# Kernel tuning notes

Measured on AMD Instinct MI355X. Metric: run time of the kernel, lower is better.

## Reference

```python
import jax, jax.numpy as jnp
import numpy as np

N_NODES = 100000
N_EDGES = 1600000
D_FEAT = 128
HIDDEN = 16
N_CLASSES = 16


def setup_inputs() -> dict:
    key = jax.random.key(0)
    ks = jax.random.split(key, 6)
    x = jax.random.normal(ks[0], (N_NODES, D_FEAT), dtype=jnp.float32)
    edge_index = jax.random.randint(ks[1], (2, N_EDGES), 0, N_NODES, dtype=jnp.int64)
    # Glorot-ish scaled weights
    w1_rel = jax.random.normal(ks[2], (D_FEAT, HIDDEN), dtype=jnp.float32) / np.sqrt(D_FEAT)
    w1_root = jax.random.normal(ks[3], (D_FEAT, HIDDEN), dtype=jnp.float32) / np.sqrt(D_FEAT)
    b1 = jnp.zeros((HIDDEN,), dtype=jnp.float32)
    w2_rel = jax.random.normal(ks[4], (HIDDEN, N_CLASSES), dtype=jnp.float32) / np.sqrt(HIDDEN)
    w2_root = jax.random.normal(ks[5], (HIDDEN, N_CLASSES), dtype=jnp.float32) / np.sqrt(HIDDEN)
    b2 = jnp.zeros((N_CLASSES,), dtype=jnp.float32)
    return {"x": x, "edge_index": edge_index, "w1_rel": w1_rel, "w1_root": w1_root,
            "b1": b1, "w2_rel": w2_rel, "w2_root": w2_root, "b2": b2}


def _graph_conv(x, src, dst, w_rel, w_root, b):
    # PyG GraphConv(aggr='add'): out_i = lin_rel(sum_{j->i} x_j) + lin_root(x_i)
    n = x.shape[0]
    agg = jax.ops.segment_sum(x[src], dst, num_segments=n)  # [N, d_in]
    return agg @ w_rel + x @ w_root + b


def reference(x, edge_index, w1_rel, w1_root, b1, w2_rel, w2_root, b2):
    src, dst = edge_index[0], edge_index[1]
    h = jax.nn.relu(_graph_conv(x, src, dst, w1_rel, w1_root, b1))
    # F.dropout(training=False) -> identity in eval mode
    out = _graph_conv(h, src, dst, w2_rel, w2_root, b2)
    return jax.nn.log_softmax(out, axis=1)
```

## Files before the change

### kernel.cpp

```cpp
#include <hip/hip_runtime.h>

#define DFEAT 128
#define HID 16
#define BKT_NODES 128
#define BKT_SHIFT 7
#define CAP 2432
#define CAPI 5
#define CHUNK 8192
#define NOEDGE 0xFFFFFFFFu

typedef __attribute__((ext_vector_type(8))) short short8;
typedef __attribute__((ext_vector_type(4))) float floatx4;

__device__ __forceinline__ float bf2f(unsigned v) { return __uint_as_float(v << 16); }
__device__ __forceinline__ unsigned short f2bf(float f) {
    unsigned u = __float_as_uint(f);
    return (unsigned short)((u + 0x7FFFu + ((u >> 16) & 1u)) >> 16);
}
__device__ __forceinline__ unsigned pack2(float a, float b) {
    return (unsigned)f2bf(a) | ((unsigned)f2bf(b) << 16);
}

__global__ __launch_bounds__(512) void k_detect(const unsigned short* __restrict__ x,
                                                const int* __restrict__ ei,
                                                int* __restrict__ flags,
                                                int* __restrict__ gcur, int nbkt) {
    const int t = threadIdx.x;
    for (int i = t; i < nbkt; i += 512) gcur[i] = 0;
    if (t < 64) {
        unsigned short v = x[2 * t];
        int e = (v >> 7) & 0xFF;
        bool okbf = (v == 0) || (e >= 110 && e <= 130);
        unsigned long long mbf = __ballot(okbf);
        bool z = (ei[2 * t + 1] == 0);
        unsigned long long mz = __ballot(z);
        if (t == 0) {
            flags[0] = (__popcll(mbf) >= 52) ? 1 : 0;
            flags[1] = (__popcll(mz) >= 60) ? 1 : 0;
        }
    }
}

__global__ __launch_bounds__(512) void k_pl(const int* __restrict__ ei,
                                            unsigned* __restrict__ eb,
                                            int* __restrict__ gcur,
                                            const void* __restrict__ xv,
                                            const void* __restrict__ wrel,
                                            const void* __restrict__ wroot,
                                            unsigned short* __restrict__ p1b,
                                            unsigned short* __restrict__ q1b,
                                            const int* __restrict__ flags,
                                            int E, int nbkt, int N, int nPart) {
    __shared__ int hist[1024];
    const int t = threadIdx.x;

    if ((int)blockIdx.x < nPart) {
        for (int i = t; i < nbkt; i += 512) hist[i] = 0;
        __syncthreads();
        const int base = blockIdx.x * CHUNK;
        const int i64 = flags[1];
        unsigned pk[16];
        unsigned bkrk[16];
        if (i64 && !(E & 1)) {
#pragma unroll
            for (int ip = 0; ip < 8; ++ip) {
                int e = base + ip * 1024 + 2 * t;
                if (e < E) {
                    int4 sv = *(const int4*)(ei + 2 * (size_t)e);
                    int4 dv = *(const int4*)(ei + 2 * ((size_t)E + e));
                    int b0 = dv.x >> BKT_SHIFT;
                    pk[2 * ip] = ((unsigned)sv.x << BKT_SHIFT) | (unsigned)(dv.x & (BKT_NODES - 1));
                    int r0 = atomicAdd(&hist[b0], 1);
                    bkrk[2 * ip] = ((unsigned)b0 << 13) | (unsigned)r0;
                    int b1 = dv.z >> BKT_SHIFT;
                    pk[2 * ip + 1] = ((unsigned)sv.z << BKT_SHIFT) | (unsigned)(dv.z & (BKT_NODES - 1));
                    int r1 = atomicAdd(&hist[b1], 1);
                    bkrk[2 * ip + 1] = ((unsigned)b1 << 13) | (unsigned)r1;
                } else {
                    bkrk[2 * ip] = NOEDGE;
                    bkrk[2 * ip + 1] = NOEDGE;
                }
            }
        } else {
#pragma unroll
            for (int i = 0; i < 16; ++i) {
                int e = base + i * 512 + t;
                if (e < E) {
                    int src, dst;
                    if (i64) { src = ei[2 * (size_t)e]; dst = ei[2 * ((size_t)E + e)]; }
                    else     { src = ei[e];             dst = ei[(size_t)E + e]; }
                    int b = dst >> BKT_SHIFT;
                    pk[i] = ((unsigned)src << BKT_SHIFT) | (unsigned)(dst & (BKT_NODES - 1));
                    int r = atomicAdd(&hist[b], 1);
                    bkrk[i] = ((unsigned)b << 13) | (unsigned)r;
                } else {
                    bkrk[i] = NOEDGE;
                }
            }
        }
        __syncthreads();
        for (int b = t; b < nbkt; b += 512) {
            int c = hist[b];
            hist[b] = c ? atomicAdd(&gcur[b], c) : 0;
        }
        __syncthreads();
#pragma unroll
        for (int i = 0; i < 16; ++i) {
            if (bkrk[i] != NOEDGE) {
                int b = (int)(bkrk[i] >> 13);
                int pos = hist[b] + (int)(bkrk[i] & 0x1FFFu);
                if (pos < CAP)
                    eb[(size_t)b * CAP + pos] = pk[i];
            }
        }
        return;
    }

    const int lane = t & 63, wave = t >> 6;
    const int bf = flags[0];
    const int m = lane & 15;
    const int quad = lane >> 4;
    const int nodebase = ((int)blockIdx.x - nPart) * 128 + wave * 16;

    short8 Brel[4], Broot[4];
    if (bf) {
        const unsigned short* a = (const unsigned short*)wrel;
        const unsigned short* c = (const unsigned short*)wroot;
#pragma unroll
        for (int kb = 0; kb < 4; ++kb) {
            short8 br, bo;
#pragma unroll
            for (int j = 0; j < 8; ++j) {
                int k = kb * 32 + quad * 8 + j;
                br[j] = (short)a[k * HID + m];
                bo[j] = (short)c[k * HID + m];
            }
            Brel[kb] = br; Broot[kb] = bo;
        }
    } else {
        const float* a = (const float*)wrel;
        const float* c = (const float*)wroot;
#pragma unroll
        for (int kb = 0; kb < 4; ++kb) {
            short8 br, bo;
#pragma unroll
            for (int j = 0; j < 8; ++j) {
                int k = kb * 32 + quad * 8 + j;
                br[j] = (short)f2bf(a[k * HID + m]);
                bo[j] = (short)f2bf(c[k * HID + m]);
            }
            Brel[kb] = br; Broot[kb] = bo;
        }
    }

    int row = nodebase + m;
    if (row >= N) row = N - 1;

    floatx4 accP = {0.f, 0.f, 0.f, 0.f}, accQ = {0.f, 0.f, 0.f, 0.f};
    if (bf) {
        const unsigned short* xp = (const unsigned short*)xv;
        const unsigned short* rp = xp + (size_t)row * DFEAT + quad * 8;
#pragma unroll
        for (int kb = 0; kb < 4; ++kb) {
            short8 A = *(const short8*)(rp + kb * 32);
            accP = __builtin_amdgcn_mfma_f32_16x16x32_bf16(A, Brel[kb], accP, 0, 0, 0);
            accQ = __builtin_amdgcn_mfma_f32_16x16x32_bf16(A, Broot[kb], accQ, 0, 0, 0);
        }
    } else {
        const float* xp = (const float*)xv;
        const float* rp = xp + (size_t)row * DFEAT + quad * 8;
#pragma unroll
        for (int kb = 0; kb < 4; ++kb) {
            float4 v0 = *(const float4*)(rp + kb * 32);
            float4 v1 = *(const float4*)(rp + kb * 32 + 4);
            short8 A;
            A[0] = (short)f2bf(v0.x); A[1] = (short)f2bf(v0.y);
            A[2] = (short)f2bf(v0.z); A[3] = (short)f2bf(v0.w);
            A[4] = (short)f2bf(v1.x); A[5] = (short)f2bf(v1.y);
            A[6] = (short)f2bf(v1.z); A[7] = (short)f2bf(v1.w);
            accP = __builtin_amdgcn_mfma_f32_16x16x32_bf16(A, Brel[kb], accP, 0, 0, 0);
            accQ = __builtin_amdgcn_mfma_f32_16x16x32_bf16(A, Broot[kb], accQ, 0, 0, 0);
        }
    }

#pragma unroll
    for (int r = 0; r < 4; ++r) {
        int node = nodebase + quad * 4 + r;
        if (node < N) {
            p1b[(size_t)node * HID + m] = f2bf(accP[r]);
            q1b[(size_t)node * HID + m] = f2bf(accQ[r]);
        }
    }
}

__global__ __launch_bounds__(512) void k_sagg1(const unsigned* __restrict__ eb,
                                               const int* __restrict__ gcur,
                                               const unsigned short* __restrict__ p1b,
                                               const unsigned short* __restrict__ q1b,
                                               const void* __restrict__ b1,
                                               const void* __restrict__ w2rel,
                                               const void* __restrict__ w2root,
                                               unsigned short* __restrict__ p2b,
                                               unsigned short* __restrict__ q2b,
                                               unsigned* __restrict__ csr,
                                               int* __restrict__ offsets,
                                               const int* __restrict__ flags,
                                               int N) {
    __shared__ unsigned srt[CAP];
    __shared__ int cnts[BKT_NODES];
    __shared__ int offs[BKT_NODES];
    __shared__ float4 swpR[HID][4];
    __shared__ float4 swpO[HID][4];
    __shared__ float sb[HID];
    const int t = threadIdx.x;
    const int b = blockIdx.x;
    const int bf = flags[0];

    if (t < 64) {
        int k = t >> 2, p = t & 3;
        float4 wr, wo;
        if (bf) {
            const unsigned short* a = (const unsigned short*)w2rel;
            const unsigned short* c = (const unsigned short*)w2root;
            wr = make_float4(bf2f(a[k * 16 + 4 * p]),     bf2f(a[k * 16 + 4 * p + 1]),
                             bf2f(a[k * 16 + 4 * p + 2]), bf2f(a[k * 16 + 4 * p + 3]));
            wo = make_float4(bf2f(c[k * 16 + 4 * p]),     bf2f(c[k * 16 + 4 * p + 1]),
                             bf2f(c[k * 16 + 4 * p + 2]), bf2f(c[k * 16 + 4 * p + 3]));
        } else {
            const float* a = (const float*)w2rel;
            const float* c = (const float*)w2root;
            wr = make_float4(a[k * 16 + 4 * p], a[k * 16 + 4 * p + 1],
                             a[k * 16 + 4 * p + 2], a[k * 16 + 4 * p + 3]);
            wo = make_float4(c[k * 16 + 4 * p], c[k * 16 + 4 * p + 1],
                             c[k * 16 + 4 * p + 2], c[k * 16 + 4 * p + 3]);
        }
        swpR[k][p] = wr;
        swpO[k][p] = wo;
    }
    if (t < HID) sb[t] = bf ? bf2f(((const unsigned short*)b1)[t]) : ((const float*)b1)[t];
    if (t < BKT_NODES) cnts[t] = 0;
    __syncthreads();

    int cnt = gcur[b];
    if (cnt < 0) cnt = 0;
    if (cnt > CAP) cnt = CAP;
    const unsigned* ep = eb + (size_t)b * CAP;

    unsigned ev[CAPI];
    int rk[CAPI];
#pragma unroll
    for (int i = 0; i < CAPI; ++i) {
        int e = i * 512 + t;
        if (e < cnt) {
            unsigned w = ep[e];
            ev[i] = w;
            rk[i] = atomicAdd(&cnts[w & (BKT_NODES - 1u)], 1);
        } else ev[i] = NOEDGE;
    }
    __syncthreads();
    if (t < BKT_NODES) offs[t] = cnts[t];
    __syncthreads();
    for (int off = 1; off < BKT_NODES; off <<= 1) {
        int v = 0;
        if (t >= off && t < BKT_NODES) v = offs[t - off];
        __syncthreads();
        if (t < BKT_NODES) offs[t] += v;
        __syncthreads();
    }
#pragma unroll
    for (int i = 0; i < CAPI; ++i) {
        if (ev[i] != NOEDGE) {
            unsigned local = ev[i] & (BKT_NODES - 1u);
            int pos = offs[local] - cnts[local] + rk[i];
            srt[pos] = ev[i] >> BKT_SHIFT;
        }
    }
    __syncthreads();

    const int base = b * CAP;
    for (int e = t; e < cnt; e += 512) csr[base + e] = srt[e];
    const int gb = b * BKT_NODES;
    if (t < BKT_NODES) {
        int gn = gb + t;
        if (gn < N) offsets[gn] = base + offs[t] - cnts[t];
    }

    const int node = t >> 2, jp = t & 3;
    const int gn = gb + node;
    const int beg = offs[node] - cnts[node];
    const int end = offs[node];
    float a0 = 0.f, a1 = 0.f, a2 = 0.f, a3 = 0.f;
    int e = beg;
    for (; e + 8 <= end; e += 8) {
        uint2 u0 = *(const uint2*)(p1b + (size_t)srt[e + 0] * HID + 4 * jp);
        uint2 u1 = *(const uint2*)(p1b + (size_t)srt[e + 1] * HID + 4 * jp);
        uint2 u2 = *(const uint2*)(p1b + (size_t)srt[e + 2] * HID + 4 * jp);
        uint2 u3 = *(const uint2*)(p1b + (size_t)srt[e + 3] * HID + 4 * jp);
        uint2 u4 = *(const uint2*)(p1b + (size_t)srt[e + 4] * HID + 4 * jp);
        uint2 u5 = *(const uint2*)(p1b + (size_t)srt[e + 5] * HID + 4 * jp);
        uint2 u6 = *(const uint2*)(p1b + (size_t)srt[e + 6] * HID + 4 * jp);
        uint2 u7 = *(const uint2*)(p1b + (size_t)srt[e + 7] * HID + 4 * jp);
        a0 += bf2f(u0.x & 0xFFFFu) + bf2f(u1.x & 0xFFFFu) + bf2f(u2.x & 0xFFFFu) + bf2f(u3.x & 0xFFFFu)
            + bf2f(u4.x & 0xFFFFu) + bf2f(u5.x & 0xFFFFu) + bf2f(u6.x & 0xFFFFu) + bf2f(u7.x & 0xFFFFu);
        a1 += bf2f(u0.x >> 16) + bf2f(u1.x >> 16) + bf2f(u2.x >> 16) + bf2f(u3.x >> 16)
            + bf2f(u4.x >> 16) + bf2f(u5.x >> 16) + bf2f(u6.x >> 16) + bf2f(u7.x >> 16);
        a2 += bf2f(u0.y & 0xFFFFu) + bf2f(u1.y & 0xFFFFu) + bf2f(u2.y & 0xFFFFu) + bf2f(u3.y & 0xFFFFu)
            + bf2f(u4.y & 0xFFFFu) + bf2f(u5.y & 0xFFFFu) + bf2f(u6.y & 0xFFFFu) + bf2f(u7.y & 0xFFFFu);
        a3 += bf2f(u0.y >> 16) + bf2f(u1.y >> 16) + bf2f(u2.y >> 16) + bf2f(u3.y >> 16)
            + bf2f(u4.y >> 16) + bf2f(u5.y >> 16) + bf2f(u6.y >> 16) + bf2f(u7.y >> 16);
    }
    for (; e + 2 <= end; e += 2) {
        uint2 u0 = *(const uint2*)(p1b + (size_t)srt[e] * HID + 4 * jp);
        uint2 u1 = *(const uint2*)(p1b + (size_t)srt[e + 1] * HID + 4 * jp);
        a0 += bf2f(u0.x & 0xFFFFu) + bf2f(u1.x & 0xFFFFu);
        a1 += bf2f(u0.x >> 16) + bf2f(u1.x >> 16);
        a2 += bf2f(u0.y & 0xFFFFu) + bf2f(u1.y & 0xFFFFu);
        a3 += bf2f(u0.y >> 16) + bf2f(u1.y >> 16);
    }
    for (; e < end; ++e) {
        uint2 u = *(const uint2*)(p1b + (size_t)srt[e] * HID + 4 * jp);
        a0 += bf2f(u.x & 0xFFFFu);
        a1 += bf2f(u.x >> 16);
        a2 += bf2f(u.y & 0xFFFFu);
        a3 += bf2f(u.y >> 16);
    }
    float h0 = 0.f, h1 = 0.f, h2 = 0.f, h3 = 0.f;
    if (gn < N) {
        uint2 qu = *(const uint2*)(q1b + (size_t)gn * HID + 4 * jp);
        h0 = fmaxf(a0 + bf2f(qu.x & 0xFFFFu) + sb[4 * jp], 0.f);
        h1 = fmaxf(a1 + bf2f(qu.x >> 16)     + sb[4 * jp + 1], 0.f);
        h2 = fmaxf(a2 + bf2f(qu.y & 0xFFFFu) + sb[4 * jp + 2], 0.f);
        h3 = fmaxf(a3 + bf2f(qu.y >> 16)     + sb[4 * jp + 3], 0.f);
    }
    float p0 = 0.f, p1 = 0.f, p2 = 0.f, p3 = 0.f;
    float q0 = 0.f, q1 = 0.f, q2 = 0.f, q3 = 0.f;
#pragma unroll
    for (int k = 0; k < HID; ++k) {
        float hsel = ((k & 3) == 0) ? h0 : ((k & 3) == 1) ? h1 : ((k & 3) == 2) ? h2 : h3;
        float hk = __shfl(hsel, k >> 2, 4);
        float4 wr = swpR[k][jp];
        float4 wo = swpO[k][jp];
        p0 += hk * wr.x; p1 += hk * wr.y; p2 += hk * wr.z; p3 += hk * wr.w;
        q0 += hk * wo.x; q1 += hk * wo.y; q2 += hk * wo.z; q3 += hk * wo.w;
    }
    if (gn < N) {
        uint2 pv; pv.x = pack2(p0, p1); pv.y = pack2(p2, p3);
        uint2 qv; qv.x = pack2(q0, q1); qv.y = pack2(q2, q3);
        ((uint2*)p2b)[(size_t)gn * 4 + jp] = pv;
        ((uint2*)q2b)[(size_t)gn * 4 + jp] = qv;
    }
}

__global__ __launch_bounds__(512) void k_agg2(const int* __restrict__ offsets,
                                              const int* __restrict__ gcur,
                                              const unsigned* __restrict__ csr,
                                              const unsigned short* __restrict__ p2b,
                                              const unsigned short* __restrict__ q2b,
                                              const void* __restrict__ b2,
                                              void* __restrict__ out,
                                              const int* __restrict__ flags,
                                              int N) {
    __shared__ unsigned srt[CAP];
    __shared__ float sb[HID];
    const int t = threadIdx.x;
    const int b = blockIdx.x;
    const int bf = flags[0];
    if (t < HID) sb[t] = bf ? bf2f(((const unsigned short*)b2)[t]) : ((const float*)b2)[t];

    int cnt = gcur[b];
    if (cnt < 0) cnt = 0;
    if (cnt > CAP) cnt = CAP;
    const int base = b * CAP;
    for (int e = t; e < cnt; e += 512) srt[e] = csr[base + e];
    __syncthreads();

    const int gb = b * BKT_NODES;
    const int node = t >> 2, jp = t & 3;
    const int gn = gb + node;
    int beg = 0, end = 0;
    if (gn < N) {
        beg = offsets[gn] - base;
        end = (node == BKT_NODES - 1 || gn + 1 >= N) ? cnt : offsets[gn + 1] - base;
    }
    float a0 = 0.f, a1 = 0.f, a2 = 0.f, a3 = 0.f;
    int e = beg;
    for (; e + 8 <= end; e += 8) {
        uint2 u0 = *(const uint2*)(p2b + (size_t)srt[e + 0] * HID + 4 * jp);
        uint2 u1 = *(const uint2*)(p2b + (size_t)srt[e + 1] * HID + 4 * jp);
        uint2 u2 = *(const uint2*)(p2b + (size_t)srt[e + 2] * HID + 4 * jp);
        uint2 u3 = *(const uint2*)(p2b + (size_t)srt[e + 3] * HID + 4 * jp);
        uint2 u4 = *(const uint2*)(p2b + (size_t)srt[e + 4] * HID + 4 * jp);
        uint2 u5 = *(const uint2*)(p2b + (size_t)srt[e + 5] * HID + 4 * jp);
        uint2 u6 = *(const uint2*)(p2b + (size_t)srt[e + 6] * HID + 4 * jp);
        uint2 u7 = *(const uint2*)(p2b + (size_t)srt[e + 7] * HID + 4 * jp);
        a0 += bf2f(u0.x & 0xFFFFu) + bf2f(u1.x & 0xFFFFu) + bf2f(u2.x & 0xFFFFu) + bf2f(u3.x & 0xFFFFu)
            + bf2f(u4.x & 0xFFFFu) + bf2f(u5.x & 0xFFFFu) + bf2f(u6.x & 0xFFFFu) + bf2f(u7.x & 0xFFFFu);
        a1 += bf2f(u0.x >> 16) + bf2f(u1.x >> 16) + bf2f(u2.x >> 16) + bf2f(u3.x >> 16)
            + bf2f(u4.x >> 16) + bf2f(u5.x >> 16) + bf2f(u6.x >> 16) + bf2f(u7.x >> 16);
        a2 += bf2f(u0.y & 0xFFFFu) + bf2f(u1.y & 0xFFFFu) + bf2f(u2.y & 0xFFFFu) + bf2f(u3.y & 0xFFFFu)
            + bf2f(u4.y & 0xFFFFu) + bf2f(u5.y & 0xFFFFu) + bf2f(u6.y & 0xFFFFu) + bf2f(u7.y & 0xFFFFu);
        a3 += bf2f(u0.y >> 16) + bf2f(u1.y >> 16) + bf2f(u2.y >> 16) + bf2f(u3.y >> 16)
            + bf2f(u4.y >> 16) + bf2f(u5.y >> 16) + bf2f(u6.y >> 16) + bf2f(u7.y >> 16);
    }
    for (; e + 2 <= end; e += 2) {
        uint2 u0 = *(const uint2*)(p2b + (size_t)srt[e] * HID + 4 * jp);
        uint2 u1 = *(const uint2*)(p2b + (size_t)srt[e + 1] * HID + 4 * jp);
        a0 += bf2f(u0.x & 0xFFFFu) + bf2f(u1.x & 0xFFFFu);
        a1 += bf2f(u0.x >> 16) + bf2f(u1.x >> 16);
        a2 += bf2f(u0.y & 0xFFFFu) + bf2f(u1.y & 0xFFFFu);
        a3 += bf2f(u0.y >> 16) + bf2f(u1.y >> 16);
    }
    for (; e < end; ++e) {
        uint2 u = *(const uint2*)(p2b + (size_t)srt[e] * HID + 4 * jp);
        a0 += bf2f(u.x & 0xFFFFu);
        a1 += bf2f(u.x >> 16);
        a2 += bf2f(u.y & 0xFFFFu);
        a3 += bf2f(u.y >> 16);
    }
    float o0 = 0.f, o1 = 0.f, o2 = 0.f, o3 = 0.f;
    if (gn < N) {
        uint2 qu = *(const uint2*)(q2b + (size_t)gn * HID + 4 * jp);
        o0 = a0 + bf2f(qu.x & 0xFFFFu) + sb[4 * jp];
        o1 = a1 + bf2f(qu.x >> 16)     + sb[4 * jp + 1];
        o2 = a2 + bf2f(qu.y & 0xFFFFu) + sb[4 * jp + 2];
        o3 = a3 + bf2f(qu.y >> 16)     + sb[4 * jp + 3];
    }
    float m = fmaxf(fmaxf(o0, o1), fmaxf(o2, o3));
    m = fmaxf(m, __shfl_xor(m, 1, 4));
    m = fmaxf(m, __shfl_xor(m, 2, 4));
    float s = __expf(o0 - m) + __expf(o1 - m) + __expf(o2 - m) + __expf(o3 - m);
    s += __shfl_xor(s, 1, 4);
    s += __shfl_xor(s, 2, 4);
    const float l = m + __logf(s);
    if (gn < N) {
        if (bf) {
            uint2 ov; ov.x = pack2(o0 - l, o1 - l); ov.y = pack2(o2 - l, o3 - l);
            ((uint2*)out)[(size_t)gn * 4 + jp] = ov;
        } else {
            ((float4*)out)[(size_t)gn * 4 + jp] =
                make_float4(o0 - l, o1 - l, o2 - l, o3 - l);
        }
    }
}

extern "C" void kernel_launch(void* const* d_in, const int* in_sizes, int n_in,
                              void* d_out, int out_size, void* d_ws, size_t ws_size,
                              hipStream_t stream) {
    const void* x       = d_in[0];
    const int*  ei      = (const int*)d_in[1];
    const void* w1_rel  = d_in[2];
    const void* w1_root = d_in[3];
    const void* b1      = d_in[4];
    const void* w2_rel  = d_in[5];
    const void* w2_root = d_in[6];
    const void* b2      = d_in[7];

    const int N = in_sizes[0] / DFEAT;
    const int E = in_sizes[1] / 2;
    const int nbkt = (N + BKT_NODES - 1) / BKT_NODES;

    unsigned short* p1b = (unsigned short*)d_ws;
    unsigned short* q1b = p1b + (size_t)N * HID;
    unsigned short* p2b = q1b + (size_t)N * HID;
    unsigned short* q2b = p2b + (size_t)N * HID;
    unsigned* eb   = (unsigned*)(q2b + (size_t)N * HID);
    unsigned* csr  = eb + (size_t)nbkt * CAP;
    int* offsets   = (int*)(csr + (size_t)nbkt * CAP);
    int* gcur      = offsets + N;
    int* flags     = gcur + nbkt;

    const int nPart = (E + CHUNK - 1) / CHUNK;
    const int nLin  = (N + 127) / 128;

    k_detect<<<1, 512, 0, stream>>>((const unsigned short*)x, ei, flags, gcur, nbkt);
    k_pl<<<nPart + nLin, 512, 0, stream>>>(ei, eb, gcur, x, w1_rel, w1_root,
                                           p1b, q1b, flags, E, nbkt, N, nPart);
    k_sagg1<<<nbkt, 512, 0, stream>>>(eb, gcur, p1b, q1b, b1, w2_rel, w2_root,
                                      p2b, q2b, csr, offsets, flags, N);
    k_agg2<<<nbkt, 512, 0, stream>>>(offsets, gcur, csr, p2b, q2b, b2,
                                     d_out, flags, N);
}
```

Measured before the change: 154.4 us.

## Recompute per-bucket sort in layer-2 aggregation instead of storing CSR; halve partition chunk

The first aggregation kernel no longer writes a sorted CSR array and per-node offsets to global memory. The second aggregation kernel re-reads the raw bucketed edge list and redoes the shared-memory counting sort itself. This trades one global write plus one global read of the edge array for repeated LDS atomics and a prefix scan in the second kernel. The partition chunk is also halved, which doubles the number of partition blocks and halves the per-thread edge registers.

```diff
diff --git a/kernel.cpp b/kernel.cpp
--- a/kernel.cpp
+++ b/kernel.cpp
@@ -6,7 +6,7 @@
 #define BKT_SHIFT 7
 #define CAP 2432
 #define CAPI 5
-#define CHUNK 8192
+#define CHUNK 4096
 #define NOEDGE 0xFFFFFFFFu
 
 typedef __attribute__((ext_vector_type(8))) short short8;
@@ -59,11 +59,11 @@
         __syncthreads();
         const int base = blockIdx.x * CHUNK;
         const int i64 = flags[1];
-        unsigned pk[16];
-        unsigned bkrk[16];
+        unsigned pk[8];
+        unsigned bkrk[8];
         if (i64 && !(E & 1)) {
 #pragma unroll
-            for (int ip = 0; ip < 8; ++ip) {
+            for (int ip = 0; ip < 4; ++ip) {
                 int e = base + ip * 1024 + 2 * t;
                 if (e < E) {
                     int4 sv = *(const int4*)(ei + 2 * (size_t)e);
@@ -83,7 +83,7 @@
             }
         } else {
 #pragma unroll
-            for (int i = 0; i < 16; ++i) {
+            for (int i = 0; i < 8; ++i) {
                 int e = base + i * 512 + t;
                 if (e < E) {
                     int src, dst;
@@ -105,7 +105,7 @@
         }
         __syncthreads();
 #pragma unroll
-        for (int i = 0; i < 16; ++i) {
+        for (int i = 0; i < 8; ++i) {
             if (bkrk[i] != NOEDGE) {
                 int b = (int)(bkrk[i] >> 13);
                 int pos = hist[b] + (int)(bkrk[i] & 0x1FFFu);
@@ -202,8 +202,6 @@
                                                const void* __restrict__ w2root,
                                                unsigned short* __restrict__ p2b,
                                                unsigned short* __restrict__ q2b,
-                                               unsigned* __restrict__ csr,
-                                               int* __restrict__ offsets,
                                                const int* __restrict__ flags,
                                                int N) {
     __shared__ unsigned srt[CAP];
@@ -277,14 +275,7 @@
     }
     __syncthreads();
 
-    const int base = b * CAP;
-    for (int e = t; e < cnt; e += 512) csr[base + e] = srt[e];
     const int gb = b * BKT_NODES;
-    if (t < BKT_NODES) {
-        int gn = gb + t;
-        if (gn < N) offsets[gn] = base + offs[t] - cnts[t];
-    }
-
     const int node = t >> 2, jp = t & 3;
     const int gn = gb + node;
     const int beg = offs[node] - cnts[node];
@@ -351,9 +342,8 @@
     }
 }
 
-__global__ __launch_bounds__(512) void k_agg2(const int* __restrict__ offsets,
+__global__ __launch_bounds__(512) void k_agg2(const unsigned* __restrict__ eb,
                                               const int* __restrict__ gcur,
-                                              const unsigned* __restrict__ csr,
                                               const unsigned short* __restrict__ p2b,
                                               const unsigned short* __restrict__ q2b,
                                               const void* __restrict__ b2,
@@ -361,27 +351,57 @@
                                               const int* __restrict__ flags,
                                               int N) {
     __shared__ unsigned srt[CAP];
+    __shared__ int cnts[BKT_NODES];
+    __shared__ int offs[BKT_NODES];
     __shared__ float sb[HID];
     const int t = threadIdx.x;
     const int b = blockIdx.x;
     const int bf = flags[0];
     if (t < HID) sb[t] = bf ? bf2f(((const unsigned short*)b2)[t]) : ((const float*)b2)[t];
+    if (t < BKT_NODES) cnts[t] = 0;
+    __syncthreads();
 
     int cnt = gcur[b];
     if (cnt < 0) cnt = 0;
     if (cnt > CAP) cnt = CAP;
-    const int base = b * CAP;
-    for (int e = t; e < cnt; e += 512) srt[e] = csr[base + e];
+    const unsigned* ep = eb + (size_t)b * CAP;
+
+    unsigned ev[CAPI];
+    int rk[CAPI];
+#pragma unroll
+    for (int i = 0; i < CAPI; ++i) {
+        int e = i * 512 + t;
+        if (e < cnt) {
+            unsigned w = ep[e];
+            ev[i] = w;
+            rk[i] = atomicAdd(&cnts[w & (BKT_NODES - 1u)], 1);
+        } else ev[i] = NOEDGE;
+    }
+    __syncthreads();
+    if (t < BKT_NODES) offs[t] = cnts[t];
+    __syncthreads();
+    for (int off = 1; off < BKT_NODES; off <<= 1) {
+        int v = 0;
+        if (t >= off && t < BKT_NODES) v = offs[t - off];
+        __syncthreads();
+        if (t < BKT_NODES) offs[t] += v;
+        __syncthreads();
+    }
+#pragma unroll
+    for (int i = 0; i < CAPI; ++i) {
+        if (ev[i] != NOEDGE) {
+            unsigned local = ev[i] & (BKT_NODES - 1u);
+            int pos = offs[local] - cnts[local] + rk[i];
+            srt[pos] = ev[i] >> BKT_SHIFT;
+        }
+    }
     __syncthreads();
 
     const int gb = b * BKT_NODES;
     const int node = t >> 2, jp = t & 3;
     const int gn = gb + node;
-    int beg = 0, end = 0;
-    if (gn < N) {
-        beg = offsets[gn] - base;
-        end = (node == BKT_NODES - 1 || gn + 1 >= N) ? cnt : offsets[gn + 1] - base;
-    }
+    const int beg = offs[node] - cnts[node];
+    const int end = offs[node];
     float a0 = 0.f, a1 = 0.f, a2 = 0.f, a3 = 0.f;
     int e = beg;
     for (; e + 8 <= end; e += 8) {
@@ -464,9 +484,7 @@
     unsigned short* p2b = q1b + (size_t)N * HID;
     unsigned short* q2b = p2b + (size_t)N * HID;
     unsigned* eb   = (unsigned*)(q2b + (size_t)N * HID);
-    unsigned* csr  = eb + (size_t)nbkt * CAP;
-    int* offsets   = (int*)(csr + (size_t)nbkt * CAP);
-    int* gcur      = offsets + N;
+    int* gcur      = (int*)(eb + (size_t)nbkt * CAP);
     int* flags     = gcur + nbkt;
 
     const int nPart = (E + CHUNK - 1) / CHUNK;
@@ -476,7 +494,6 @@
     k_pl<<<nPart + nLin, 512, 0, stream>>>(ei, eb, gcur, x, w1_rel, w1_root,
                                            p1b, q1b, flags, E, nbkt, N, nPart);
     k_sagg1<<<nbkt, 512, 0, stream>>>(eb, gcur, p1b, q1b, b1, w2_rel, w2_root,
-                                      p2b, q2b, csr, offsets, flags, N);
-    k_agg2<<<nbkt, 512, 0, stream>>>(offsets, gcur, csr, p2b, q2b, b2,
-                                     d_out, flags, N);
-}
+                                      p2b, q2b, flags, N);
+    k_agg2<<<nbkt, 512, 0, stream>>>(eb, gcur, p2b, q2b, b2, d_out, flags, N);
+}
```

Result: slower. 161.7 us (+4.8%).
